# Kernel optimization log

Hardware: AMD Instinct MI355X
Metric: run time of the kernel (lower is better)

## Reference

```python
import jax, jax.numpy as jnp
import numpy as np

B, S, D, H, HD = 1, 4096, 768, 12, 64
L, C, WIN, NCLS = 2, 256, 256, 64
NC = S // C
V, FF = 50265, 3072
NEG = -1e9
SCALE = np.float32(1.0 / np.sqrt(HD))


def setup_inputs() -> dict:
    key = jax.random.key(0)
    ks = jax.random.split(key, 32)
    p = lambda k, shape: (0.02 * jax.random.normal(k, shape)).astype(jnp.float32)
    inp = {
        'x': jax.random.randint(ks[0], (B, S), 0, V, dtype=jnp.int32),
        'mask_src': jnp.ones((B, S), dtype=jnp.int32),
        'clss': jnp.sort(jax.random.randint(ks[1], (B, NCLS), 0, S, dtype=jnp.int32), axis=-1),
        'segs': jax.random.randint(ks[2], (B, S), 0, 2, dtype=jnp.int32),
        'word_emb': p(ks[3], (V, D)),
        'pos_emb': p(ks[4], (S, D)),
        'type_emb': p(ks[5], (2, D)),
        'ln_e_s': jnp.ones((D,), jnp.float32), 'ln_e_b': jnp.zeros((D,), jnp.float32),
        'Wq': p(ks[6], (L, D, D)), 'bq': jnp.zeros((L, D), jnp.float32),
        'Wk': p(ks[7], (L, D, D)), 'bk': jnp.zeros((L, D), jnp.float32),
        'Wv': p(ks[8], (L, D, D)), 'bv': jnp.zeros((L, D), jnp.float32),
        'Wqg': p(ks[9], (L, D, D)), 'bqg': jnp.zeros((L, D), jnp.float32),
        'Wkg': p(ks[10], (L, D, D)), 'bkg': jnp.zeros((L, D), jnp.float32),
        'Wvg': p(ks[11], (L, D, D)), 'bvg': jnp.zeros((L, D), jnp.float32),
        'Wo': p(ks[12], (L, D, D)), 'bo': jnp.zeros((L, D), jnp.float32),
        'ln1_s': jnp.ones((L, D), jnp.float32), 'ln1_b': jnp.zeros((L, D), jnp.float32),
        'Wf1': p(ks[13], (L, D, FF)), 'bf1': jnp.zeros((L, FF), jnp.float32),
        'Wf2': p(ks[14], (L, FF, D)), 'bf2': jnp.zeros((L, D), jnp.float32),
        'ln2_s': jnp.ones((L, D), jnp.float32), 'ln2_b': jnp.zeros((L, D), jnp.float32),
    }
    return inp


def _layer_norm(x, s, b):
    m = jnp.mean(x, -1, keepdims=True)
    v = jnp.mean((x - m) ** 2, -1, keepdims=True)
    return (x - m) * jax.lax.rsqrt(v + 1e-5) * s + b


def _forward(x, mask_src, clss, segs, word_emb, pos_emb, type_emb, ln_e_s, ln_e_b,
             Wq, bq, Wk, bk, Wv, bv, Wqg, bqg, Wkg, bkg, Wvg, bvg, Wo, bo,
             ln1_s, ln1_b, Wf1, bf1, Wf2, bf2, ln2_s, ln2_b):
    # global positions: union of all clss values, same for every batch row
    g_idx = clss.reshape(-1)                                       # [NCLS]
    is_glb = jnp.zeros((S,), bool).at[g_idx].set(True)             # [S]
    kvalid = (mask_src > 0) & (~is_glb)[None, :]                   # band keys: no pad, no global
    gi = (jnp.arange(NC) * C)[:, None] + jnp.arange(3 * C)[None, :]  # gather idx into padded seq
    rel = jnp.arange(3 * C)[None, :] - (jnp.arange(C)[:, None] + C)  # key offset from query
    band_ok = jnp.abs(rel) <= WIN                                   # [C,3C]
    kv3 = jnp.pad(kvalid, ((0, 0), (C, C)))[:, gi]                  # [B,NC,3C]
    bmask = band_ok[None, None, None, :, :] & kv3[:, None, :, None, :]  # [B,1,NC,C,3C]
    gkey_ok = (mask_src[:, g_idx] > 0)[:, None, None, :]            # [B,1,1,NCLS]
    full_ok = (mask_src > 0)[:, None, None, :]                      # [B,1,1,S]

    h = _layer_norm(word_emb[x] + pos_emb[jnp.arange(S)][None] + type_emb[segs], ln_e_s, ln_e_b)

    for l in range(L):
        q = ((h @ Wq[l] + bq[l]).reshape(B, S, H, HD)) * SCALE
        k = (h @ Wk[l] + bk[l]).reshape(B, S, H, HD)
        v = (h @ Wv[l] + bv[l]).reshape(B, S, H, HD)
        # --- sliding-window band attention ---
        k3 = jnp.pad(k, ((0, 0), (C, C), (0, 0), (0, 0)))[:, gi]    # [B,NC,3C,H,HD]
        v3 = jnp.pad(v, ((0, 0), (C, C), (0, 0), (0, 0)))[:, gi]
        qc = q.reshape(B, NC, C, H, HD)
        sb = jnp.einsum('bnqhd,bnkhd->bhnqk', qc, k3)               # [B,H,NC,C,3C]
        sb = jnp.where(bmask, sb, NEG)
        # --- global keys seen by every query ---
        kg, vg = k[:, g_idx], v[:, g_idx]                           # [B,NCLS,H,HD]
        sg = jnp.einsum('bshd,bkhd->bhsk', q, kg)                   # [B,H,S,NCLS]
        sg = jnp.where(gkey_ok, sg, NEG)
        scores = jnp.concatenate([sg, sb.reshape(B, H, S, 3 * C)], -1)
        probs = jax.nn.softmax(scores, axis=-1)
        pg = probs[..., :NCLS]
        pb = probs[..., NCLS:].reshape(B, H, NC, C, 3 * C)
        out = jnp.einsum('bhnqk,bnkhd->bnqhd', pb, v3).reshape(B, S, H, HD)
        out = out + jnp.einsum('bhsk,bkhd->bshd', pg, vg)
        # --- global query tokens: full attention with *_global projections ---
        hg = h[:, g_idx]                                            # [B,NCLS,D]
        qg = ((hg @ Wqg[l] + bqg[l]).reshape(B, NCLS, H, HD)) * SCALE
        kgf = (h @ Wkg[l] + bkg[l]).reshape(B, S, H, HD)
        vgf = (h @ Wvg[l] + bvg[l]).reshape(B, S, H, HD)
        sfull = jnp.einsum('bqhd,bkhd->bhqk', qg, kgf)              # [B,H,NCLS,S]
        sfull = jnp.where(full_ok, sfull, NEG)
        og = jnp.einsum('bhqk,bkhd->bqhd', jax.nn.softmax(sfull, -1), vgf)
        out = out.at[:, g_idx].set(og)
        # --- output proj, residual, LN, FFN ---
        attn_out = out.reshape(B, S, D) @ Wo[l] + bo[l]
        h = _layer_norm(h + attn_out, ln1_s[l], ln1_b[l])
        ff = jax.nn.gelu(h @ Wf1[l] + bf1[l]) @ Wf2[l] + bf2[l]
        h = _layer_norm(h + ff, ln2_s[l], ln2_b[l])
    return h


def reference(x, mask_src, clss, segs, word_emb, pos_emb, type_emb, ln_e_s, ln_e_b,
              Wq, bq, Wk, bk, Wv, bv, Wqg, bqg, Wkg, bkg, Wvg, bvg, Wo, bo,
              ln1_s, ln1_b, Wf1, bf1, Wf2, bf2, ln2_s, ln2_b):
    return _forward(x, mask_src, clss, segs, word_emb, pos_emb, type_emb, ln_e_s, ln_e_b,
                    Wq, bq, Wk, bk, Wv, bv, Wqg, bqg, Wkg, bkg, Wvg, bvg, Wo, bo,
                    ln1_s, ln1_b, Wf1, bf1, Wf2, bf2, ln2_s, ln2_b)
```

## Files before the change

kernel.cpp:

```cpp
#include <hip/hip_runtime.h>
#include <hip/hip_bf16.h>
#include <cstdint>

#define SEQ  4096
#define DIM  768
#define NH   12
#define HDIM 64
#define NLAYER 2
#define CHK  256
#define WINR 256
#define NCLS 64
#define NCHK 16
#define FFD  3072
#define QSCALE 0.125f
#define LOG2E 1.44269504f
#define QSC2 (QSCALE * LOG2E)
#define SD ((size_t)SEQ * DIM)
#define PS_LD 72
#define TK 64

typedef __attribute__((__vector_size__(16))) float floatx4;
typedef __attribute__((ext_vector_type(8))) __bf16 bf16x8;
typedef __attribute__((ext_vector_type(4))) __bf16 bf16x4;

__device__ __forceinline__ void async16(const void* g, void* l) {
    __builtin_amdgcn_global_load_lds(
        (const __attribute__((address_space(1))) uint32_t*)g,
        (__attribute__((address_space(3))) uint32_t*)l, 16, 0, 0);
}

__device__ __forceinline__ float gelu_f(float x) {
    float x3 = x * x * x;
    return 0.5f * x * (1.0f + tanhf(0.7978845608028654f * (x + 0.044715f * x3)));
}

__global__ __launch_bounds__(64) void set_rank_kernel(
    const int* __restrict__ clss, int* __restrict__ isglb, int* __restrict__ glb_rank)
{
    int t = threadIdx.x;
    int p = clss[t];
    isglb[p] = 1;
    glb_rank[p] = t;
}

__global__ __launch_bounds__(256) void embed_ln_kernel(
    const int* __restrict__ x, const int* __restrict__ segs,
    const float* __restrict__ word_emb, const float* __restrict__ pos_emb,
    const float* __restrict__ type_emb, const float* __restrict__ gs,
    const float* __restrict__ gb, float* __restrict__ h, __bf16* __restrict__ hb,
    int* __restrict__ isglb, int* __restrict__ grank)
{
    int wave = threadIdx.x >> 6, lane = threadIdx.x & 63;
    int s = blockIdx.x * 4 + wave;
    if (lane == 0) { isglb[s] = 0; grank[s] = -1; }
    int w = x[s], sg = segs[s];
    const float4* wp = (const float4*)(word_emb + (size_t)w * DIM);
    const float4* pp = (const float4*)(pos_emb + (size_t)s * DIM);
    const float4* tp = (const float4*)(type_emb + (size_t)sg * DIM);
    float4 v[3]; float lsum = 0.f;
    #pragma unroll
    for (int i = 0; i < 3; i++) {
        int d4 = lane + i * 64;
        float4 a = wp[d4], b = pp[d4], c = tp[d4];
        float4 r;
        r.x = a.x + b.x + c.x; r.y = a.y + b.y + c.y;
        r.z = a.z + b.z + c.z; r.w = a.w + b.w + c.w;
        v[i] = r; lsum += r.x + r.y + r.z + r.w;
    }
    #pragma unroll
    for (int st = 32; st > 0; st >>= 1) lsum += __shfl_xor(lsum, st);
    float mean = lsum * (1.0f / DIM);
    float lv = 0.f;
    #pragma unroll
    for (int i = 0; i < 3; i++) {
        float dx = v[i].x - mean, dy = v[i].y - mean, dz = v[i].z - mean, dw = v[i].w - mean;
        lv += dx * dx + dy * dy + dz * dz + dw * dw;
    }
    #pragma unroll
    for (int st = 32; st > 0; st >>= 1) lv += __shfl_xor(lv, st);
    float rstd = rsqrtf(lv * (1.0f / DIM) + 1e-5f);
    #pragma unroll
    for (int i = 0; i < 3; i++) {
        int d4 = lane + i * 64;
        float4 s4v = ((const float4*)gs)[d4], b4v = ((const float4*)gb)[d4];
        float4 o;
        o.x = (v[i].x - mean) * rstd * s4v.x + b4v.x;
        o.y = (v[i].y - mean) * rstd * s4v.y + b4v.y;
        o.z = (v[i].z - mean) * rstd * s4v.z + b4v.z;
        o.w = (v[i].w - mean) * rstd * s4v.w + b4v.w;
        ((float4*)(h + (size_t)s * DIM))[d4] = o;
        bf16x4 ob; ob[0] = (__bf16)o.x; ob[1] = (__bf16)o.y;
        ob[2] = (__bf16)o.z; ob[3] = (__bf16)o.w;
        *(bf16x4*)(hb + (size_t)s * DIM + (size_t)d4 * 4) = ob;
    }
}

__global__ __launch_bounds__(256) void add_ln_kernel(
    const float* __restrict__ h, const float* __restrict__ r,
    const float* __restrict__ gs, const float* __restrict__ gb,
    float* __restrict__ hout, __bf16* __restrict__ hb)
{
    int wave = threadIdx.x >> 6, lane = threadIdx.x & 63;
    int s = blockIdx.x * 4 + wave;
    const float4* hp = (const float4*)(h + (size_t)s * DIM);
    const float4* rp = (const float4*)(r + (size_t)s * DIM);
    float4 v[3]; float lsum = 0.f;
    #pragma unroll
    for (int i = 0; i < 3; i++) {
        int d4 = lane + i * 64;
        float4 a = hp[d4], b = rp[d4];
        float4 q;
        q.x = a.x + b.x; q.y = a.y + b.y; q.z = a.z + b.z; q.w = a.w + b.w;
        v[i] = q; lsum += q.x + q.y + q.z + q.w;
    }
    #pragma unroll
    for (int st = 32; st > 0; st >>= 1) lsum += __shfl_xor(lsum, st);
    float mean = lsum * (1.0f / DIM);
    float lv = 0.f;
    #pragma unroll
    for (int i = 0; i < 3; i++) {
        float dx = v[i].x - mean, dy = v[i].y - mean, dz = v[i].z - mean, dw = v[i].w - mean;
        lv += dx * dx + dy * dy + dz * dz + dw * dw;
    }
    #pragma unroll
    for (int st = 32; st > 0; st >>= 1) lv += __shfl_xor(lv, st);
    float rstd = rsqrtf(lv * (1.0f / DIM) + 1e-5f);
    #pragma unroll
    for (int i = 0; i < 3; i++) {
        int d4 = lane + i * 64;
        float4 s4v = ((const float4*)gs)[d4], b4v = ((const float4*)gb)[d4];
        float4 o;
        o.x = (v[i].x - mean) * rstd * s4v.x + b4v.x;
        o.y = (v[i].y - mean) * rstd * s4v.y + b4v.y;
        o.z = (v[i].z - mean) * rstd * s4v.z + b4v.z;
        o.w = (v[i].w - mean) * rstd * s4v.w + b4v.w;
        ((float4*)(hout + (size_t)s * DIM))[d4] = o;
        bf16x4 ob; ob[0] = (__bf16)o.x; ob[1] = (__bf16)o.y;
        ob[2] = (__bf16)o.z; ob[3] = (__bf16)o.w;
        *(bf16x4*)(hb + (size_t)s * DIM + (size_t)d4 * 4) = ob;
    }
}

struct TArgs { const float* p14[14]; const float* f1[2]; const float* f2[2]; };
#define DD_ ((size_t)DIM * DIM)
__global__ __launch_bounds__(256) void tpose_setup_kernel(
// ... 9 lines not shown
        const float* s = (j == 0) ? bq : (j == 1) ? bk : (j == 2) ? bv : (j == 3) ? bkg : bvg;
        bqkv[idx] = s[l * 768 + d];
        return;
    }
    const float* src; __bf16* dst; int K, N, bx, by;
    if (b < 8064) {
        int z = b / 576, rr = b % 576;
        src = ta.p14[z]; dst = Wbf + (size_t)z * DD_;
        K = 768; N = 768; bx = (rr % 24) * 32; by = (rr / 24) * 32;
    } else if (b < 12672) {
        int bb = b - 8064; int z = bb / 2304, rr = bb % 2304;
        src = ta.f1[z]; dst = Wbf + 14 * DD_ + (size_t)z * 4 * DD_;
        K = 768; N = 3072; bx = (rr % 96) * 32; by = (rr / 96) * 32;
    } else {
        int bb = b - 12672; int z = bb / 2304, rr = bb % 2304;
        src = ta.f2[z]; dst = Wbf + 22 * DD_ + (size_t)z * 4 * DD_;
        K = 3072; N = 768; bx = (rr % 24) * 32; by = (rr / 24) * 32;
    }
    __shared__ float tile[32][33];
    int tx = threadIdx.x & 31, ty = threadIdx.x >> 5;
    #pragma unroll
    for (int i = 0; i < 32; i += 8)
        tile[ty + i][tx] = src[(size_t)(by + ty + i) * N + bx + tx];
    __syncthreads();
    #pragma unroll
    for (int i = 0; i < 32; i += 8)
        dst[(size_t)(bx + ty + i) * K + by + tx] = (__bf16)tile[tx][ty + i];
}

template<int TMv, int TNv>
__global__ __launch_bounds__(256) void mfma_gemm_t(
    const __bf16* __restrict__ A, const __bf16* __restrict__ Bt,
    const float* __restrict__ bias, float* __restrict__ Cf,
    __bf16* __restrict__ Cb, int M, int N, int K, float scale, int act)
{
    constexpr int AM = TMv / 32, AN = TNv / 32;
    constexpr int LA = TMv / 32, LB = TNv / 32;
    __shared__ __align__(16) __bf16 As[TMv * TK];
    __shared__ __align__(16) __bf16 Bs[TNv * TK];
    int t = threadIdx.x;
    int wave = t >> 6, lane = t & 63;
    int bm = blockIdx.x * TMv, bn = blockIdx.y * TNv;
    int wm = (wave & 1) * (TMv / 2), wn = (wave >> 1) * (TNv / 2);

    floatx4 acc[AM][AN];
    #pragma unroll
    for (int i = 0; i < AM; i++)
        #pragma unroll
        for (int j = 0; j < AN; j++) { floatx4 z = {0.f,0.f,0.f,0.f}; acc[i][j] = z; }

    const int mrow = lane & 15, kq = (lane >> 4) * 8;
    const int tr8 = lane >> 3, c8 = lane & 7;
    const int scol = (c8 ^ tr8) * 8;
    const int swz = (lane & 7) << 3;
    const __bf16* aBase = A  + (size_t)(bm + wave * 8 + tr8) * K + scol;
    const __bf16* bBase = Bt + (size_t)(bn + wave * 8 + tr8) * K + scol;

    for (int k0 = 0; k0 < K; k0 += TK) {
        __syncthreads();
        #pragma unroll
        for (int i = 0; i < LA; i++)
            async16(aBase + k0 + (size_t)i * 32 * K, &As[(size_t)(i * 256 + wave * 64) * 8]);
        #pragma unroll
        for (int i = 0; i < LB; i++)
            async16(bBase + k0 + (size_t)i * 32 * K, &Bs[(size_t)(i * 256 + wave * 64) * 8]);
        __builtin_amdgcn_s_waitcnt(0x0f70);
        __syncthreads();
        #pragma unroll
        for (int ks = 0; ks < 2; ks++) {
            const int e = (ks * 32 + kq) ^ swz;
            bf16x8 af[AM], bfr[AN];
            #pragma unroll
            for (int mt = 0; mt < AM; mt++)
                af[mt] = *(const bf16x8*)&As[(wm + mt * 16 + mrow) * TK + e];
            #pragma unroll
            for (int nt = 0; nt < AN; nt++)
                bfr[nt] = *(const bf16x8*)&Bs[(wn + nt * 16 + mrow) * TK + e];
            #pragma unroll
            for (int mt = 0; mt < AM; mt++)
                #pragma unroll
                for (int nt = 0; nt < AN; nt++)
                    acc[mt][nt] = __builtin_amdgcn_mfma_f32_16x16x32_bf16(
                        af[mt], bfr[nt], acc[mt][nt], 0, 0, 0);
        }
    }

    int col_l = lane & 15, row_l = (lane >> 4) * 4;
    #pragma unroll
    for (int nt = 0; nt < AN; nt++) {
        int col = bn + wn + nt * 16 + col_l;
        float bs = bias[col];
        #pragma unroll
        for (int mt = 0; mt < AM; mt++) {
            floatx4 v = acc[mt][nt];
            int row0 = bm + wm + mt * 16 + row_l;
            #pragma unroll
            for (int rr = 0; rr < 4; rr++) {
                float o = (v[rr] + bs) * scale;
                if (act) o = gelu_f(o);
                if (Cf) Cf[(size_t)(row0 + rr) * N + col] = o;
                if (Cb) Cb[(size_t)(row0 + rr) * N + col] = (__bf16)o;
            }
        }
    }
}

__global__ __launch_bounds__(256) void mfma_gemm_proj(
    const __bf16* __restrict__ A, const __bf16* __restrict__ Bt,
    const float* __restrict__ bias,
    __bf16* __restrict__ qb, __bf16* __restrict__ kb,
    __bf16* __restrict__ vb, __bf16* __restrict__ vtg,
    __bf16* __restrict__ kgb, __bf16* __restrict__ vgt, int K)
{
    __shared__ __align__(16) __bf16 As[128 * TK];
    __shared__ __align__(16) __bf16 Bs[128 * TK];
    int t = threadIdx.x;
    int wave = t >> 6, lane = t & 63;
    int bm = blockIdx.x * 128, bn = blockIdx.y * 128;
    int wm = (wave & 1) * 64, wn = (wave >> 1) * 64;

    floatx4 acc[4][4];
    #pragma unroll
    for (int i = 0; i < 4; i++)
        #pragma unroll
        for (int j = 0; j < 4; j++) { floatx4 z = {0.f,0.f,0.f,0.f}; acc[i][j] = z; }

    const int mrow = lane & 15, kq = (lane >> 4) * 8;
    const int tr8 = lane >> 3, c8 = lane & 7;
    const int scol = (c8 ^ tr8) * 8;
    const int swz = (lane & 7) << 3;
    const __bf16* aBase = A  + (size_t)(bm + wave * 8 + tr8) * K + scol;
    const __bf16* bBase = Bt + (size_t)(bn + wave * 8 + tr8) * K + scol;

    for (int k0 = 0; k0 < K; k0 += TK) {
        __syncthreads();
        #pragma unroll
        for (int i = 0; i < 4; i++) {
            async16(aBase + k0 + (size_t)i * 32 * K, &As[(size_t)(i * 256 + wave * 64) * 8]);
            async16(bBase + k0 + (size_t)i * 32 * K, &Bs[(size_t)(i * 256 + wave * 64) * 8]);
        }
        __builtin_amdgcn_s_waitcnt(0x0f70);
        __syncthreads();
        #pragma unroll
        for (int ks = 0; ks < 2; ks++) {
            const int e = (ks * 32 + kq) ^ swz;
            bf16x8 af[4], bfr[4];
            #pragma unroll
            for (int mt = 0; mt < 4; mt++)
                af[mt] = *(const bf16x8*)&As[(wm + mt * 16 + mrow) * TK + e];
            #pragma unroll
            for (int nt = 0; nt < 4; nt++)
                bfr[nt] = *(const bf16x8*)&Bs[(wn + nt * 16 + mrow) * TK + e];
            #pragma unroll
            for (int mt = 0; mt < 4; mt++)
                #pragma unroll
                for (int nt = 0; nt < 4; nt++)
                    acc[mt][nt] = __builtin_amdgcn_mfma_f32_16x16x32_bf16(
                        af[mt], bfr[nt], acc[mt][nt], 0, 0, 0);
        }
    }

    int col_l = lane & 15, row_l = (lane >> 4) * 4;
    int seg = bn / 768;
    int colw_base = bn - seg * 768 + wn;
    float scl = (seg == 0) ? QSC2 : 1.0f;
    #pragma unroll
    for (int nt = 0; nt < 4; nt++) {
        int col = bn + wn + nt * 16 + col_l;
        int colw = colw_base + nt * 16 + col_l;
        float bs = bias[col];
        #pragma unroll
        for (int mt = 0; mt < 4; mt++) {
            floatx4 v = acc[mt][nt];
            int row0 = bm + wm + mt * 16 + row_l;
            __bf16 t4[4];
            #pragma unroll
            for (int rr = 0; rr < 4; rr++) t4[rr] = (__bf16)((v[rr] + bs) * scl);
            if (seg <= 2 || seg == 3) {
                __bf16* dst = (seg == 0) ? qb : (seg == 1) ? kb : (seg == 2) ? vb : kgb;
                #pragma unroll
                for (int rr = 0; rr < 4; rr++)
                    dst[(size_t)(row0 + rr) * 768 + colw] = t4[rr];
            }
            if (seg == 2)
                *(uint2*)&vtg[(size_t)colw * SEQ + row0] = *(uint2*)t4;
            if (seg == 4)
                *(uint2*)&vgt[(size_t)colw * SEQ + row0] = *(uint2*)t4;
        }
    }
}

__global__ __launch_bounds__(256) void qg_proj(
    const __bf16* __restrict__ hb, const __bf16* __restrict__ Bt,
    const int* __restrict__ clss, const float* __restrict__ bias,
    __bf16* __restrict__ out)
{
    __shared__ __align__(16) __bf16 As[64 * TK];
    __shared__ __align__(16) __bf16 Bs[128 * TK];
    int t = threadIdx.x;
    int wave = t >> 6, lane = t & 63;
    int bn = blockIdx.y * 128;
    int wm = (wave & 1) * 32, wn = (wave >> 1) * 64;

    const int mrow = lane & 15, kq = (lane >> 4) * 8;
    const int tr8 = lane >> 3, c8 = lane & 7;
    const int scol = (c8 ^ tr8) * 8;
    const int swz = (lane & 7) << 3;
    int arow0 = wave * 8 + tr8;
    int g0 = clss[arow0], g1 = clss[32 + arow0];
    const __bf16* a0 = hb + (size_t)g0 * DIM + scol;
    const __bf16* a1 = hb + (size_t)g1 * DIM + scol;
    const __bf16* bBase = Bt + (size_t)(bn + wave * 8 + tr8) * DIM + scol;

    floatx4 acc[2][4];
    #pragma unroll
    for (int i = 0; i < 2; i++)
        #pragma unroll
        for (int j = 0; j < 4; j++) { floatx4 z = {0.f,0.f,0.f,0.f}; acc[i][j] = z; }

    for (int k0 = 0; k0 < DIM; k0 += TK) {
        __syncthreads();
        async16(a0 + k0, &As[(size_t)(wave * 64) * 8]);
        async16(a1 + k0, &As[(size_t)(256 + wave * 64) * 8]);
        #pragma unroll
        for (int i = 0; i < 4; i++)
            async16(bBase + k0 + (size_t)i * 32 * DIM, &Bs[(size_t)(i * 256 + wave * 64) * 8]);
        __builtin_amdgcn_s_waitcnt(0x0f70);
        __syncthreads();
        #pragma unroll
        for (int ks = 0; ks < 2; ks++) {
            const int e = (ks * 32 + kq) ^ swz;
            bf16x8 af[2], bfr[4];
            #pragma unroll
            for (int mt = 0; mt < 2; mt++)
                af[mt] = *(const bf16x8*)&As[(wm + mt * 16 + mrow) * TK + e];
            #pragma unroll
            for (int nt = 0; nt < 4; nt++)
                bfr[nt] = *(const bf16x8*)&Bs[(wn + nt * 16 + mrow) * TK + e];
            #pragma unroll
            for (int mt = 0; mt < 2; mt++)
                #pragma unroll
                for (int nt = 0; nt < 4; nt++)
                    acc[mt][nt] = __builtin_amdgcn_mfma_f32_16x16x32_bf16(
                        af[mt], bfr[nt], acc[mt][nt], 0, 0, 0);
        }
    }
    int col_l = lane & 15, row_l = (lane >> 4) * 4;
    #pragma unroll
    for (int nt = 0; nt < 4; nt++) {
        int col = bn + wn + nt * 16 + col_l;
        float bs = bias[col];
        #pragma unroll
        for (int mt = 0; mt < 2; mt++) {
            floatx4 v = acc[mt][nt];
            int row0 = wm + mt * 16 + row_l;
            #pragma unroll
            for (int rr = 0; rr < 4; rr++)
                out[(size_t)(row0 + rr) * DIM + col] = (__bf16)((v[rr] + bs) * QSC2);
        }
    }
}

__global__ __launch_bounds__(256) void attn_kernel(
    const __bf16* __restrict__ qb, const __bf16* __restrict__ kb,
    const __bf16* __restrict__ vb, const __bf16* __restrict__ vtg,
    const __bf16* __restrict__ qgbb, const __bf16* __restrict__ kgb,
    const __bf16* __restrict__ vgt,
    const int* __restrict__ clss, const int* __restrict__ mask_src,
    const int* __restrict__ is_glb,
    float* __restrict__ OpartB, float* __restrict__ mlpartB,
    float* __restrict__ OpartG, float* __restrict__ mlpartG)
{
    __shared__ __align__(16) __bf16 Kt[4096];
    __shared__ __align__(16) __bf16 Vt[4096];
    __shared__ __align__(16) __bf16 Ps[4][32 * PS_LD];
    __shared__ int kvalid[64];
    __shared__ int gpos[64];

    const int hh = blockIdx.y;
    const int t = threadIdx.x, wave = t >> 6, lane = t & 63;
    const int quad = lane >> 4, col_l = lane & 15, row_l = quad * 4;
    const int l3 = lane & 3, l2h = lane >> 2, l7 = lane & 7, l3h = lane >> 3;
    __bf16* PsW = Ps[wave];

    if (blockIdx.z >= 4) {
        const int sp = blockIdx.x * 2 + (blockIdx.z - 4);
        bf16x8 aq[2];
        {
            const __bf16* qp = qgbb + (size_t)(wave * 16 + col_l) * DIM + hh * HDIM;
            aq[0] = *(const bf16x8*)(qp + quad * 8);
            aq[1] = *(const bf16x8*)(qp + 32 + quad * 8);
        }
        floatx4 oacc[4];
        #pragma unroll
        for (int i = 0; i < 4; i++) { floatx4 z = {0.f,0.f,0.f,0.f}; oacc[i] = z; }
        float m4[4], l4[4];
        #pragma unroll
        for (int r = 0; r < 4; r++) { m4[r] = -1e30f; l4[r] = 0.f; }

        for (int tt = 0; tt < 2; tt++) {
            int pos0 = sp * 128 + tt * 64;
            __syncthreads();
            if (t < 64) kvalid[t] = (mask_src[pos0 + t] > 0) ? 1 : 0;
            #pragma unroll
            for (int ii = 0; ii < 2; ii++) {
                int gid = wave * 2 + ii;
                int p = gid >> 2, kbase = (gid & 3) * 16;
                async16(kgb + (size_t)(pos0 + kbase + l2h) * DIM + hh * HDIM + p * 32 + l3 * 8,
                        &Kt[p * 2048 + kbase * 32]);
            }
            #pragma unroll
            for (int ii = 0; ii < 2; ii++) {
                int gid = wave * 2 + ii;
                int p = gid >> 2, dbase = (gid & 3) * 16;
                async16(vgt + (size_t)(hh * HDIM + dbase + l2h) * SEQ + pos0 + p * 32 + l3 * 8,
                        &Vt[p * 2048 + dbase * 32]);
            }
            __builtin_amdgcn_s_waitcnt(0x0f70);
            __syncthreads();
// ... 37 lines not shown
                rsum += __shfl_xor(rsum, 4);
                rsum += __shfl_xor(rsum, 8);
                l4[rr] = l4[rr] * alpha + rsum;
                m4[rr] = mn;
                #pragma unroll
                for (int nt = 0; nt < 4; nt++) oacc[nt][rr] *= alpha;
            }
            bf16x8 ap0 = *(const bf16x8*)&PsW[col_l * PS_LD + quad * 8];
            bf16x8 ap1 = *(const bf16x8*)&PsW[col_l * PS_LD + 32 + quad * 8];
            #pragma unroll
            for (int nt = 0; nt < 4; nt++) {
                bf16x8 b0 = *(const bf16x8*)&Vt[(nt * 16 + col_l) * 32 + quad * 8];
                bf16x8 b1 = *(const bf16x8*)&Vt[2048 + (nt * 16 + col_l) * 32 + quad * 8];
                oacc[nt] = __builtin_amdgcn_mfma_f32_16x16x32_bf16(ap0, b0, oacc[nt], 0,0,0);
                oacc[nt] = __builtin_amdgcn_mfma_f32_16x16x32_bf16(ap1, b1, oacc[nt], 0,0,0);
            }
        }
        size_t base = (size_t)(hh * 32 + sp) * 64;
        #pragma unroll
        for (int nt = 0; nt < 4; nt++)
            #pragma unroll
            for (int rr = 0; rr < 4; rr++)
                OpartG[(base + wave * 16 + row_l + rr) * 64 + nt * 16 + col_l] = oacc[nt][rr];
        if (col_l == 0) {
            #pragma unroll
            for (int rr = 0; rr < 4; rr++) {
                mlpartG[(base + wave * 16 + row_l + rr) * 2]     = m4[rr];
                mlpartG[(base + wave * 16 + row_l + rr) * 2 + 1] = l4[rr];
            }
        }
        return;
    }

    const int n = blockIdx.x, zi = blockIdx.z;
    const int qh = zi >> 1, ks = zi & 1;
    const int qw = qh * 128 + wave * 32;

    if (t < 64) gpos[t] = clss[t];

    bf16x8 aq[2][2];
    #pragma unroll
    for (int mt = 0; mt < 2; mt++) {
        const __bf16* qp = qb + (size_t)(n * CHK + qw + mt * 16 + col_l) * DIM + hh * HDIM;
        aq[mt][0] = *(const bf16x8*)(qp + quad * 8);
        aq[mt][1] = *(const bf16x8*)(qp + 32 + quad * 8);
    }

    floatx4 oacc[2][4];
    #pragma unroll
    for (int i = 0; i < 2; i++)
        #pragma unroll
        for (int j = 0; j < 4; j++) { floatx4 z = {0.f,0.f,0.f,0.f}; oacc[i][j] = z; }
    float mrw[8], lrw[8];
    #pragma unroll
    for (int r = 0; r < 8; r++) { mrw[r] = -1e30f; lrw[r] = 0.f; }

    const int ntiles = ks ? 5 : 6;

    for (int tt = 0; tt < ntiles; tt++) {
        __syncthreads();
        int jbase = -1;
        int isglob = (ks == 0 && tt == 0);
        if (isglob) {
            if (t < 64) kvalid[t] = (mask_src[gpos[t]] > 0) ? 1 : 0;
            #pragma unroll
            for (int g = 0; g < 2; g++) {
                int gid = wave * 2 + g;
                int p = gid >> 2, kbase = (gid & 3) * 16;
                int pos = gpos[kbase + l2h];
                async16(kb + (size_t)pos * DIM + hh * HDIM + p * 32 + l3 * 8,
                        &Kt[p * 2048 + kbase * 32]);
            }
            __bf16* Vrow = &Ps[0][0];
            #pragma unroll
            for (int g = 0; g < 2; g++) {
                int cg = wave * 2 + g;
                int pos = gpos[cg * 8 + l3h];
                async16(vb + (size_t)pos * DIM + hh * HDIM + l7 * 8,
                        &Vrow[cg * 64 * 8]);
            }
        } else {
            int jt = ks ? (qh * 2 + 5 + tt) : (qh * 2 + tt - 1);
            jbase = jt * 64;
            if (t < 64) {
                int pos = n * CHK + jbase + t - CHK;
                kvalid[t] = (pos >= 0 && pos < SEQ && mask_src[pos] > 0
                             && is_glb[pos] == 0) ? 1 : 0;
            }
            int s0 = n * CHK + jbase - CHK;
            #pragma unroll
            for (int g = 0; g < 2; g++) {
                int gid = wave * 2 + g;
                int p = gid >> 2, kbase = (gid & 3) * 16;
                int pos = s0 + kbase + l2h; pos = min(max(pos, 0), SEQ - 1);
                async16(kb + (size_t)pos * DIM + hh * HDIM + p * 32 + l3 * 8,
                        &Kt[p * 2048 + kbase * 32]);
            }
            #pragma unroll
            for (int g = 0; g < 2; g++) {
                int gid = wave * 2 + g;
                int p = gid >> 2, dbase = (gid & 3) * 16;
                int d = dbase + l2h;
                int s = s0 + p * 32 + l3 * 8; s = min(max(s, 0), SEQ - 8);
                async16(vtg + (size_t)(hh * HDIM + d) * SEQ + s,
                        &Vt[p * 2048 + dbase * 32]);
            }
        }
        __builtin_amdgcn_s_waitcnt(0x0f70);
        __syncthreads();
        if (isglob) {
            const __bf16* Vrow = &Ps[0][0];
            for (int idx = t; idx < 4096; idx += 256) {
                int key = idx >> 6, d = idx & 63;
                Vt[(key >> 5) * 2048 + d * 32 + (key & 31)] = Vrow[idx];
            }
// ... 59 lines not shown
                lrw[ri] = lrw[ri] * alpha + rsum;
                mrw[ri] = mn;
                #pragma unroll
                for (int nt = 0; nt < 4; nt++) oacc[mt][nt][rr] *= alpha;
            }
        }
        bf16x8 bvf[4][2], ap[2][2];
        #pragma unroll
        for (int nt = 0; nt < 4; nt++) {
            bvf[nt][0] = *(const bf16x8*)&Vt[(nt * 16 + col_l) * 32 + quad * 8];
            bvf[nt][1] = *(const bf16x8*)&Vt[2048 + (nt * 16 + col_l) * 32 + quad * 8];
        }
        #pragma unroll
        for (int mt = 0; mt < 2; mt++) {
            ap[mt][0] = *(const bf16x8*)&PsW[(mt * 16 + col_l) * PS_LD + quad * 8];
            ap[mt][1] = *(const bf16x8*)&PsW[(mt * 16 + col_l) * PS_LD + 32 + quad * 8];
        }
        #pragma unroll
        for (int mt = 0; mt < 2; mt++)
            #pragma unroll
            for (int nt = 0; nt < 4; nt++) {
                oacc[mt][nt] = __builtin_amdgcn_mfma_f32_16x16x32_bf16(
                    ap[mt][0], bvf[nt][0], oacc[mt][nt], 0,0,0);
                oacc[mt][nt] = __builtin_amdgcn_mfma_f32_16x16x32_bf16(
                    ap[mt][1], bvf[nt][1], oacc[mt][nt], 0,0,0);
            }
    }

    #pragma unroll
    for (int mt = 0; mt < 2; mt++) {
        #pragma unroll
        for (int rr = 0; rr < 4; rr++) {
            int srow = n * CHK + qw + mt * 16 + row_l + rr;
            size_t rbase = ((size_t)ks * SEQ + srow) * NH + hh;
            #pragma unroll
            for (int nt = 0; nt < 4; nt++)
                OpartB[rbase * 64 + nt * 16 + col_l] = oacc[mt][nt][rr];
            if (col_l == 0) {
                mlpartB[rbase * 2]     = mrw[mt * 4 + rr];
                mlpartB[rbase * 2 + 1] = lrw[mt * 4 + rr];
            }
        }
    }
}

__global__ __launch_bounds__(256) void attn_finalize(
    const float* __restrict__ OpartB, const float* __restrict__ mlpartB,
    const float* __restrict__ OpartG, const float* __restrict__ mlpartG,
    const int* __restrict__ glb_rank, __bf16* __restrict__ outb)
{
    int g = threadIdx.x >> 6, d = threadIdx.x & 63;
    int s = blockIdx.x * 4 + g, hh = blockIdx.y;
    int r = glb_rank[s];
    float o;
    if (r >= 0) {
        float M = -1e30f;
        for (int sp = 0; sp < 32; sp++)
            M = fmaxf(M, mlpartG[(((size_t)hh * 32 + sp) * 64 + r) * 2]);
        float L = 0.f, acc = 0.f;
        for (int sp = 0; sp < 32; sp++) {
            size_t b = ((size_t)hh * 32 + sp) * 64 + r;
            float w = exp2f(mlpartG[b * 2] - M);
            L += mlpartG[b * 2 + 1] * w;
            acc += w * OpartG[b * 64 + d];
        }
        o = acc / L;
    } else {
        size_t r0 = ((size_t)s) * NH + hh;
        size_t r1 = ((size_t)SEQ + s) * NH + hh;
        float m0 = mlpartB[r0 * 2], l0 = mlpartB[r0 * 2 + 1];
        float m1 = mlpartB[r1 * 2], l1 = mlpartB[r1 * 2 + 1];
        float M = fmaxf(m0, m1);
        float w0 = exp2f(m0 - M), w1 = exp2f(m1 - M);
        o = (OpartB[r0 * 64 + d] * w0 + OpartB[r1 * 64 + d] * w1) / (l0 * w0 + l1 * w1);
    }
    outb[(size_t)s * DIM + hh * HDIM + d] = (__bf16)o;
}

extern "C" void kernel_launch(void* const* d_in, const int* in_sizes, int n_in,
                              void* d_out, int out_size, void* d_ws, size_t ws_size,
                              hipStream_t stream)
{
    const int* x        = (const int*)d_in[0];
    const int* mask_src = (const int*)d_in[1];
    const int* clss     = (const int*)d_in[2];
    const int* segs     = (const int*)d_in[3];
    const float* word_emb = (const float*)d_in[4];
    const float* pos_emb  = (const float*)d_in[5];
    const float* type_emb = (const float*)d_in[6];
    const float* ln_e_s   = (const float*)d_in[7];
    const float* ln_e_b   = (const float*)d_in[8];
    const float* Wq  = (const float*)d_in[9];
    const float* bq  = (const float*)d_in[10];
    const float* Wk  = (const float*)d_in[11];
    const float* bk  = (const float*)d_in[12];
    const float* Wv  = (const float*)d_in[13];
    const float* bv  = (const float*)d_in[14];
    const float* Wqg = (const float*)d_in[15];
    const float* bqg = (const float*)d_in[16];
    const float* Wkg = (const float*)d_in[17];
    const float* bkg = (const float*)d_in[18];
    const float* Wvg = (const float*)d_in[19];
    const float* bvg = (const float*)d_in[20];
    const float* Wo  = (const float*)d_in[21];
    const float* bo  = (const float*)d_in[22];
    const float* ln1_s = (const float*)d_in[23];
    const float* ln1_b = (const float*)d_in[24];
    const float* Wf1 = (const float*)d_in[25];
    const float* bf1 = (const float*)d_in[26];
    const float* Wf2 = (const float*)d_in[27];
    const float* bf2 = (const float*)d_in[28];
    const float* ln2_s = (const float*)d_in[29];
    const float* ln2_b = (const float*)d_in[30];

    const size_t DD = (size_t)DIM * DIM;
    float* ws = (float*)d_ws;
    float*  h    = ws;
    float*  s4   = ws + SD;
    __bf16* hb   = (__bf16*)(ws + 2 * SD);
    __bf16* b6b  = (__bf16*)(ws + 2 * SD) + SD;
    __bf16* qb   = (__bf16*)(ws + 3 * SD);
    __bf16* kb   = (__bf16*)(ws + 3 * SD) + SD;
    __bf16* vb   = (__bf16*)(ws + 4 * SD);
    __bf16* vtg  = (__bf16*)(ws + 4 * SD) + SD;
    __bf16* kgb  = (__bf16*)(ws + 5 * SD);
    __bf16* vgt  = (__bf16*)(ws + 5 * SD) + SD;
    __bf16* gelu_b = qb;
    float* extra = ws + 6 * SD;
    __bf16* Wbf   = (__bf16*)extra;
    float* after_w = extra + 15 * DD;
    float* bqkv   = after_w;
    float* OpartG = bqkv + 7680;
    float* mlpartG= OpartG + 1572864;
    float* OpartB = mlpartG + 49152;
    float* mlpartB= OpartB + 6291456;
    __bf16* qgbb  = (__bf16*)(mlpartB + 196608);
    int*   isglb  = (int*)(qgbb + (size_t)NCLS * DIM);
    int*   grank  = isglb + SEQ;

    embed_ln_kernel<<<SEQ / 4, 256, 0, stream>>>(x, segs, word_emb, pos_emb, type_emb,
                                                 ln_e_s, ln_e_b, h, hb, isglb, grank);
    set_rank_kernel<<<1, 64, 0, stream>>>(clss, isglb, grank);
    {
        TArgs ta{};
        ta.p14[0] = Wq;        ta.p14[1] = Wk;        ta.p14[2] = Wv;
        ta.p14[3] = Wkg;       ta.p14[4] = Wvg;
        ta.p14[5] = Wq + DD;   ta.p14[6] = Wk + DD;   ta.p14[7] = Wv + DD;
        ta.p14[8] = Wkg + DD;  ta.p14[9] = Wvg + DD;
        ta.p14[10] = Wo;       ta.p14[11] = Wo + DD;
        ta.p14[12] = Wqg;      ta.p14[13] = Wqg + DD;
        ta.f1[0] = Wf1; ta.f1[1] = Wf1 + (size_t)DIM * FFD;
        ta.f2[0] = Wf2; ta.f2[1] = Wf2 + (size_t)FFD * DIM;
        tpose_setup_kernel<<<17310, 256, 0, stream>>>(ta, Wbf, bq, bk, bv, bkg, bvg, bqkv);
    }

    for (int l = 0; l < NLAYER; l++) {
        const float* bqg_l = bqg + (size_t)l * DIM;
        const float* bo_l  = bo  + (size_t)l * DIM;
        const float* bf1_l = bf1 + (size_t)l * FFD;
        const float* bf2_l = bf2 + (size_t)l * DIM;

        qg_proj<<<dim3(1, 6), 256, 0, stream>>>(
            hb, Wbf + 12 * DD + (size_t)l * DD, clss, bqg_l, qgbb);
        mfma_gemm_proj<<<dim3(SEQ / 128, 3840 / 128), 256, 0, stream>>>(
            hb, Wbf + (size_t)l * 5 * DD, bqkv + l * 3840,
            qb, kb, vb, vtg, kgb, vgt, DIM);
        attn_kernel<<<dim3(NCHK, NH, 6), 256, 0, stream>>>(
            qb, kb, vb, vtg, qgbb, kgb, vgt, clss, mask_src, isglb,
            OpartB, mlpartB, OpartG, mlpartG);
        attn_finalize<<<dim3(SEQ / 4, NH), 256, 0, stream>>>(
            OpartB, mlpartB, OpartG, mlpartG, grank, b6b);
        mfma_gemm_t<128, 64><<<dim3(SEQ / 128, DIM / 64), 256, 0, stream>>>(
            b6b, Wbf + 10 * DD + (size_t)l * DD, bo_l, s4, nullptr,
            SEQ, DIM, DIM, 1.0f, 0);
        add_ln_kernel<<<SEQ / 4, 256, 0, stream>>>(h, s4, ln1_s + (size_t)l * DIM,
                                                   ln1_b + (size_t)l * DIM, h, hb);
        mfma_gemm_t<128, 128><<<dim3(SEQ / 128, FFD / 128), 256, 0, stream>>>(
            hb, Wbf + 14 * DD + (size_t)l * 4 * DD, bf1_l, nullptr, gelu_b,
            SEQ, FFD, DIM, 1.0f, 1);
        mfma_gemm_t<128, 64><<<dim3(SEQ / 128, DIM / 64), 256, 0, stream>>>(
            gelu_b, Wbf + 22 * DD + (size_t)l * 4 * DD, bf2_l, s4, nullptr,
            SEQ, DIM, FFD, 1.0f, 0);
        add_ln_kernel<<<SEQ / 4, 256, 0, stream>>>(h, s4, ln2_s + (size_t)l * DIM,
                                                   ln2_b + (size_t)l * DIM,
                                                   (l == NLAYER - 1) ? (float*)d_out : h, hb);
    }
}
```

Before: 783.9 us.

## Split-K output/FFN2 GEMMs, fuse qg projection and band-attention finalize

The Wo and FFN2 GEMMs are split along K into two grid-z slices. Each slice writes its own fp32 partial, and the following add+LayerNorm kernel sums both partials, which doubles the block count for these narrow-N GEMMs. The separate qg_proj launch is folded into extra blockIdx.y columns of the QKV projection kernel. Band attention no longer splits key tiles across two blocks: each block normalizes its own output and writes bf16 directly, and only global-query rows go through a small finalize kernel. This removes launches and partial buffers, at the cost of fewer, longer attention blocks and an extra fp32 partial read in the LayerNorm kernels.

Result: faster. 721.8 us (-7.9%).

```diff
diff --git a/kernel.cpp b/kernel.cpp
--- a/kernel.cpp
+++ b/kernel.cpp
@@ -35,12 +35,9 @@
 }
 
 __global__ __launch_bounds__(64) void set_rank_kernel(
-    const int* __restrict__ clss, int* __restrict__ isglb, int* __restrict__ glb_rank)
+    const int* __restrict__ clss, int* __restrict__ isglb)
 {
-    int t = threadIdx.x;
-    int p = clss[t];
-    isglb[p] = 1;
-    glb_rank[p] = t;
+    isglb[clss[threadIdx.x]] = 1;
 }
 
 __global__ __launch_bounds__(256) void embed_ln_kernel(
@@ -48,11 +45,11 @@
     const float* __restrict__ word_emb, const float* __restrict__ pos_emb,
     const float* __restrict__ type_emb, const float* __restrict__ gs,
     const float* __restrict__ gb, float* __restrict__ h, __bf16* __restrict__ hb,
-    int* __restrict__ isglb, int* __restrict__ grank)
+    int* __restrict__ isglb)
 {
     int wave = threadIdx.x >> 6, lane = threadIdx.x & 63;
     int s = blockIdx.x * 4 + wave;
-    if (lane == 0) { isglb[s] = 0; grank[s] = -1; }
+    if (lane == 0) isglb[s] = 0;
     int w = x[s], sg = segs[s];
     const float4* wp = (const float4*)(word_emb + (size_t)w * DIM);
     const float4* pp = (const float4*)(pos_emb + (size_t)s * DIM);
@@ -97,6 +94,7 @@
 
 __global__ __launch_bounds__(256) void add_ln_kernel(
     const float* __restrict__ h, const float* __restrict__ r,
+    const float* __restrict__ r2,
     const float* __restrict__ gs, const float* __restrict__ gb,
     float* __restrict__ hout, __bf16* __restrict__ hb)
 {
@@ -104,13 +102,15 @@
     int s = blockIdx.x * 4 + wave;
     const float4* hp = (const float4*)(h + (size_t)s * DIM);
     const float4* rp = (const float4*)(r + (size_t)s * DIM);
+    const float4* rp2 = (const float4*)(r2 + (size_t)s * DIM);
     float4 v[3]; float lsum = 0.f;
     #pragma unroll
     for (int i = 0; i < 3; i++) {
         int d4 = lane + i * 64;
-        float4 a = hp[d4], b = rp[d4];
+        float4 a = hp[d4], b = rp[d4], c = rp2[d4];
         float4 q;
-        q.x = a.x + b.x; q.y = a.y + b.y; q.z = a.z + b.z; q.w = a.w + b.w;
+        q.x = a.x + b.x + c.x; q.y = a.y + b.y + c.y;
+        q.z = a.z + b.z + c.z; q.w = a.w + b.w + c.w;
         v[i] = q; lsum += q.x + q.y + q.z + q.w;
     }
     #pragma unroll
@@ -186,7 +186,8 @@
 __global__ __launch_bounds__(256) void mfma_gemm_t(
     const __bf16* __restrict__ A, const __bf16* __restrict__ Bt,
     const float* __restrict__ bias, float* __restrict__ Cf,
-    __bf16* __restrict__ Cb, int M, int N, int K, float scale, int act)
+    float* __restrict__ Cf2, __bf16* __restrict__ Cb,
+    int M, int N, int K, float scale, int act)
 {
     constexpr int AM = TMv / 32, AN = TNv / 32;
     constexpr int LA = TMv / 32, LB = TNv / 32;
@@ -196,6 +197,9 @@
     int wave = t >> 6, lane = t & 63;
     int bm = blockIdx.x * TMv, bn = blockIdx.y * TNv;
     int wm = (wave & 1) * (TMv / 2), wn = (wave >> 1) * (TNv / 2);
+    int kz = blockIdx.z;
+    int kn = K / (int)gridDim.z, kbeg = kz * kn;
+    float* Cfo = (kz == 0) ? Cf : Cf2;
 
     floatx4 acc[AM][AN];
     #pragma unroll
@@ -210,7 +214,7 @@
     const __bf16* aBase = A  + (size_t)(bm + wave * 8 + tr8) * K + scol;
     const __bf16* bBase = Bt + (size_t)(bn + wave * 8 + tr8) * K + scol;
 
-    for (int k0 = 0; k0 < K; k0 += TK) {
+    for (int k0 = kbeg; k0 < kbeg + kn; k0 += TK) {
         __syncthreads();
         #pragma unroll
         for (int i = 0; i < LA; i++)
@@ -243,7 +247,7 @@
     #pragma unroll
     for (int nt = 0; nt < AN; nt++) {
         int col = bn + wn + nt * 16 + col_l;
-        float bs = bias[col];
+        float bs = (kz == 0) ? bias[col] : 0.f;
         #pragma unroll
         for (int mt = 0; mt < AM; mt++) {
             floatx4 v = acc[mt][nt];
@@ -252,7 +256,7 @@
             for (int rr = 0; rr < 4; rr++) {
                 float o = (v[rr] + bs) * scale;
                 if (act) o = gelu_f(o);
-                if (Cf) Cf[(size_t)(row0 + rr) * N + col] = o;
+                if (Cfo) Cfo[(size_t)(row0 + rr) * N + col] = o;
                 if (Cb) Cb[(size_t)(row0 + rr) * N + col] = (__bf16)o;
             }
         }
@@ -264,25 +268,88 @@
     const float* __restrict__ bias,
     __bf16* __restrict__ qb, __bf16* __restrict__ kb,
     __bf16* __restrict__ vb, __bf16* __restrict__ vtg,
-    __bf16* __restrict__ kgb, __bf16* __restrict__ vgt, int K)
+    __bf16* __restrict__ kgb, __bf16* __restrict__ vgt, int K,
+    const __bf16* __restrict__ Wqg_bt, const float* __restrict__ bqg,
+    const int* __restrict__ clss, __bf16* __restrict__ qgbb)
 {
     __shared__ __align__(16) __bf16 As[128 * TK];
     __shared__ __align__(16) __bf16 Bs[128 * TK];
     int t = threadIdx.x;
     int wave = t >> 6, lane = t & 63;
-    int bm = blockIdx.x * 128, bn = blockIdx.y * 128;
-    int wm = (wave & 1) * 64, wn = (wave >> 1) * 64;
-
-    floatx4 acc[4][4];
-    #pragma unroll
-    for (int i = 0; i < 4; i++)
-        #pragma unroll
-        for (int j = 0; j < 4; j++) { floatx4 z = {0.f,0.f,0.f,0.f}; acc[i][j] = z; }
-
     const int mrow = lane & 15, kq = (lane >> 4) * 8;
     const int tr8 = lane >> 3, c8 = lane & 7;
     const int scol = (c8 ^ tr8) * 8;
     const int swz = (lane & 7) << 3;
+    int col_l = lane & 15, row_l = (lane >> 4) * 4;
+
+    if (blockIdx.y >= 30) {
+        if (blockIdx.x != 0) return;
+        int bn = (blockIdx.y - 30) * 128;
+        int wm = (wave & 1) * 32, wn = (wave >> 1) * 64;
+        int arow0 = wave * 8 + tr8;
+        int g0 = clss[arow0], g1 = clss[32 + arow0];
+        const __bf16* a0 = A + (size_t)g0 * DIM + scol;
+        const __bf16* a1 = A + (size_t)g1 * DIM + scol;
+        const __bf16* bBase = Wqg_bt + (size_t)(bn + wave * 8 + tr8) * DIM + scol;
+
+        floatx4 acc[2][4];
+        #pragma unroll
+        for (int i = 0; i < 2; i++)
+            #pragma unroll
+            for (int j = 0; j < 4; j++) { floatx4 z = {0.f,0.f,0.f,0.f}; acc[i][j] = z; }
+
+        for (int k0 = 0; k0 < DIM; k0 += TK) {
+            __syncthreads();
+            async16(a0 + k0, &As[(size_t)(wave * 64) * 8]);
+            async16(a1 + k0, &As[(size_t)(256 + wave * 64) * 8]);
+            #pragma unroll
+            for (int i = 0; i < 4; i++)
+                async16(bBase + k0 + (size_t)i * 32 * DIM, &Bs[(size_t)(i * 256 + wave * 64) * 8]);
+            __builtin_amdgcn_s_waitcnt(0x0f70);
+            __syncthreads();
+            #pragma unroll
+            for (int ks = 0; ks < 2; ks++) {
+                const int e = (ks * 32 + kq) ^ swz;
+                bf16x8 af[2], bfr[4];
+                #pragma unroll
+                for (int mt = 0; mt < 2; mt++)
+                    af[mt] = *(const bf16x8*)&As[(wm + mt * 16 + mrow) * TK + e];
+                #pragma unroll
+                for (int nt = 0; nt < 4; nt++)
+                    bfr[nt] = *(const bf16x8*)&Bs[(wn + nt * 16 + mrow) * TK + e];
+                #pragma unroll
+                for (int mt = 0; mt < 2; mt++)
+                    #pragma unroll
+                    for (int nt = 0; nt < 4; nt++)
+                        acc[mt][nt] = __builtin_amdgcn_mfma_f32_16x16x32_bf16(
+                            af[mt], bfr[nt], acc[mt][nt], 0, 0, 0);
+            }
+        }
+        #pragma unroll
+        for (int nt = 0; nt < 4; nt++) {
+            int col = bn + wn + nt * 16 + col_l;
+            float bs = bqg[col];
+            #pragma unroll
+            for (int mt = 0; mt < 2; mt++) {
+                floatx4 v = acc[mt][nt];
+                int row0 = wm + mt * 16 + row_l;
+                #pragma unroll
+                for (int rr = 0; rr < 4; rr++)
+                    qgbb[(size_t)(row0 + rr) * DIM + col] = (__bf16)((v[rr] + bs) * QSC2);
+            }
+        }
+        return;
+    }
+
+    int bm = blockIdx.x * 128, bn = blockIdx.y * 128;
+    int wm = (wave & 1) * 64, wn = (wave >> 1) * 64;
+
+    floatx4 acc[4][4];
+    #pragma unroll
+    for (int i = 0; i < 4; i++)
+        #pragma unroll
+        for (int j = 0; j < 4; j++) { floatx4 z = {0.f,0.f,0.f,0.f}; acc[i][j] = z; }
+
     const __bf16* aBase = A  + (size_t)(bm + wave * 8 + tr8) * K + scol;
     const __bf16* bBase = Bt + (size_t)(bn + wave * 8 + tr8) * K + scol;
 
@@ -314,7 +381,6 @@
         }
     }
 
-    int col_l = lane & 15, row_l = (lane >> 4) * 4;
     int seg = bn / 768;
     int colw_base = bn - seg * 768 + wn;
     float scl = (seg == 0) ? QSC2 : 1.0f;
@@ -340,77 +406,6 @@
                 *(uint2*)&vtg[(size_t)colw * SEQ + row0] = *(uint2*)t4;
             if (seg == 4)
                 *(uint2*)&vgt[(size_t)colw * SEQ + row0] = *(uint2*)t4;
-        }
-    }
-}
-
-__global__ __launch_bounds__(256) void qg_proj(
-    const __bf16* __restrict__ hb, const __bf16* __restrict__ Bt,
-    const int* __restrict__ clss, const float* __restrict__ bias,
-    __bf16* __restrict__ out)
-{
-    __shared__ __align__(16) __bf16 As[64 * TK];
-    __shared__ __align__(16) __bf16 Bs[128 * TK];
-    int t = threadIdx.x;
-    int wave = t >> 6, lane = t & 63;
-    int bn = blockIdx.y * 128;
-    int wm = (wave & 1) * 32, wn = (wave >> 1) * 64;
-
-    const int mrow = lane & 15, kq = (lane >> 4) * 8;
-    const int tr8 = lane >> 3, c8 = lane & 7;
-    const int scol = (c8 ^ tr8) * 8;
-    const int swz = (lane & 7) << 3;
-    int arow0 = wave * 8 + tr8;
-    int g0 = clss[arow0], g1 = clss[32 + arow0];
-    const __bf16* a0 = hb + (size_t)g0 * DIM + scol;
-    const __bf16* a1 = hb + (size_t)g1 * DIM + scol;
-    const __bf16* bBase = Bt + (size_t)(bn + wave * 8 + tr8) * DIM + scol;
-
-    floatx4 acc[2][4];
-    #pragma unroll
-    for (int i = 0; i < 2; i++)
-        #pragma unroll
-        for (int j = 0; j < 4; j++) { floatx4 z = {0.f,0.f,0.f,0.f}; acc[i][j] = z; }
-
-    for (int k0 = 0; k0 < DIM; k0 += TK) {
-        __syncthreads();
-        async16(a0 + k0, &As[(size_t)(wave * 64) * 8]);
-        async16(a1 + k0, &As[(size_t)(256 + wave * 64) * 8]);
-        #pragma unroll
-        for (int i = 0; i < 4; i++)
-            async16(bBase + k0 + (size_t)i * 32 * DIM, &Bs[(size_t)(i * 256 + wave * 64) * 8]);
-        __builtin_amdgcn_s_waitcnt(0x0f70);
-        __syncthreads();
-        #pragma unroll
-        for (int ks = 0; ks < 2; ks++) {
-            const int e = (ks * 32 + kq) ^ swz;
-            bf16x8 af[2], bfr[4];
-            #pragma unroll
-            for (int mt = 0; mt < 2; mt++)
-                af[mt] = *(const bf16x8*)&As[(wm + mt * 16 + mrow) * TK + e];
-            #pragma unroll
-            for (int nt = 0; nt < 4; nt++)
-                bfr[nt] = *(const bf16x8*)&Bs[(wn + nt * 16 + mrow) * TK + e];
-            #pragma unroll
-            for (int mt = 0; mt < 2; mt++)
-                #pragma unroll
-                for (int nt = 0; nt < 4; nt++)
-                    acc[mt][nt] = __builtin_amdgcn_mfma_f32_16x16x32_bf16(
-                        af[mt], bfr[nt], acc[mt][nt], 0, 0, 0);
-        }
-    }
-    int col_l = lane & 15, row_l = (lane >> 4) * 4;
-    #pragma unroll
-    for (int nt = 0; nt < 4; nt++) {
-        int col = bn + wn + nt * 16 + col_l;
-        float bs = bias[col];
-        #pragma unroll
-        for (int mt = 0; mt < 2; mt++) {
-            floatx4 v = acc[mt][nt];
-            int row0 = wm + mt * 16 + row_l;
-            #pragma unroll
-            for (int rr = 0; rr < 4; rr++)
-                out[(size_t)(row0 + rr) * DIM + col] = (__bf16)((v[rr] + bs) * QSC2);
         }
     }
 }
@@ -422,8 +417,8 @@
     const __bf16* __restrict__ vgt,
     const int* __restrict__ clss, const int* __restrict__ mask_src,
     const int* __restrict__ is_glb,
-    float* __restrict__ OpartB, float* __restrict__ mlpartB,
-    float* __restrict__ OpartG, float* __restrict__ mlpartG)
+    float* __restrict__ OpartG, float* __restrict__ mlpartG,
+    __bf16* __restrict__ outb)
 {
     __shared__ __align__(16) __bf16 Kt[4096];
     __shared__ __align__(16) __bf16 Vt[4096];
@@ -437,8 +432,8 @@
     const int l3 = lane & 3, l2h = lane >> 2, l7 = lane & 7, l3h = lane >> 3;
     __bf16* PsW = Ps[wave];
 
-    if (blockIdx.z >= 4) {
-        const int sp = blockIdx.x * 2 + (blockIdx.z - 4);
+    if (blockIdx.z >= 2) {
+        const int sp = blockIdx.x * 2 + (blockIdx.z - 2);
         bf16x8 aq[2];
         {
             const __bf16* qp = qgbb + (size_t)(wave * 16 + col_l) * DIM + hh * HDIM;
@@ -542,8 +537,7 @@
         return;
     }
 
-    const int n = blockIdx.x, zi = blockIdx.z;
-    const int qh = zi >> 1, ks = zi & 1;
+    const int n = blockIdx.x, qh = blockIdx.z;
     const int qw = qh * 128 + wave * 32;
 
     if (t < 64) gpos[t] = clss[t];
@@ -565,12 +559,10 @@
     #pragma unroll
     for (int r = 0; r < 8; r++) { mrw[r] = -1e30f; lrw[r] = 0.f; }
 
-    const int ntiles = ks ? 5 : 6;
-
-    for (int tt = 0; tt < ntiles; tt++) {
+    for (int tt = 0; tt < 11; tt++) {
         __syncthreads();
         int jbase = -1;
-        int isglob = (ks == 0 && tt == 0);
+        int isglob = (tt == 0);
         if (isglob) {
             if (t < 64) kvalid[t] = (mask_src[gpos[t]] > 0) ? 1 : 0;
             #pragma unroll
@@ -590,7 +582,7 @@
                         &Vrow[cg * 64 * 8]);
             }
         } else {
-            int jt = ks ? (qh * 2 + 5 + tt) : (qh * 2 + tt - 1);
+            int jt = qh * 2 + tt - 1;
             jbase = jt * 64;
             if (t < 64) {
                 int pos = n * CHK + jbase + t - CHK;
@@ -716,49 +708,33 @@
         #pragma unroll
         for (int rr = 0; rr < 4; rr++) {
             int srow = n * CHK + qw + mt * 16 + row_l + rr;
-            size_t rbase = ((size_t)ks * SEQ + srow) * NH + hh;
+            if (is_glb[srow]) continue;
+            float inv = 1.0f / lrw[mt * 4 + rr];
             #pragma unroll
             for (int nt = 0; nt < 4; nt++)
-                OpartB[rbase * 64 + nt * 16 + col_l] = oacc[mt][nt][rr];
-            if (col_l == 0) {
-                mlpartB[rbase * 2]     = mrw[mt * 4 + rr];
-                mlpartB[rbase * 2 + 1] = lrw[mt * 4 + rr];
-            }
-        }
-    }
-}
-
-__global__ __launch_bounds__(256) void attn_finalize(
-    const float* __restrict__ OpartB, const float* __restrict__ mlpartB,
+                outb[(size_t)srow * DIM + hh * HDIM + nt * 16 + col_l] =
+                    (__bf16)(oacc[mt][nt][rr] * inv);
+        }
+    }
+}
+
+__global__ __launch_bounds__(64) void gq_finalize(
     const float* __restrict__ OpartG, const float* __restrict__ mlpartG,
-    const int* __restrict__ glb_rank, __bf16* __restrict__ outb)
+    const int* __restrict__ clss, __bf16* __restrict__ outb)
 {
-    int g = threadIdx.x >> 6, d = threadIdx.x & 63;
-    int s = blockIdx.x * 4 + g, hh = blockIdx.y;
-    int r = glb_rank[s];
-    float o;
-    if (r >= 0) {
-        float M = -1e30f;
-        for (int sp = 0; sp < 32; sp++)
-            M = fmaxf(M, mlpartG[(((size_t)hh * 32 + sp) * 64 + r) * 2]);
-        float L = 0.f, acc = 0.f;
-        for (int sp = 0; sp < 32; sp++) {
-            size_t b = ((size_t)hh * 32 + sp) * 64 + r;
-            float w = exp2f(mlpartG[b * 2] - M);
-            L += mlpartG[b * 2 + 1] * w;
-            acc += w * OpartG[b * 64 + d];
-        }
-        o = acc / L;
-    } else {
-        size_t r0 = ((size_t)s) * NH + hh;
-        size_t r1 = ((size_t)SEQ + s) * NH + hh;
-        float m0 = mlpartB[r0 * 2], l0 = mlpartB[r0 * 2 + 1];
-        float m1 = mlpartB[r1 * 2], l1 = mlpartB[r1 * 2 + 1];
-        float M = fmaxf(m0, m1);
-        float w0 = exp2f(m0 - M), w1 = exp2f(m1 - M);
-        o = (OpartB[r0 * 64 + d] * w0 + OpartB[r1 * 64 + d] * w1) / (l0 * w0 + l1 * w1);
-    }
-    outb[(size_t)s * DIM + hh * HDIM + d] = (__bf16)o;
+    int r = blockIdx.x, hh = blockIdx.y, d = threadIdx.x;
+    float M = -1e30f;
+    for (int sp = 0; sp < 32; sp++)
+        M = fmaxf(M, mlpartG[(((size_t)hh * 32 + sp) * 64 + r) * 2]);
+    float L = 0.f, acc = 0.f;
+    for (int sp = 0; sp < 32; sp++) {
+        size_t b = ((size_t)hh * 32 + sp) * 64 + r;
+        float w = exp2f(mlpartG[b * 2] - M);
+        L += mlpartG[b * 2 + 1] * w;
+        acc += w * OpartG[b * 64 + d];
+    }
+    int pos = clss[r];
+    outb[(size_t)pos * DIM + hh * HDIM + d] = (__bf16)(acc / L);
 }
 
 extern "C" void kernel_launch(void* const* d_in, const int* in_sizes, int n_in,
@@ -816,15 +792,13 @@
     float* bqkv   = after_w;
     float* OpartG = bqkv + 7680;
     float* mlpartG= OpartG + 1572864;
-    float* OpartB = mlpartG + 49152;
-    float* mlpartB= OpartB + 6291456;
-    __bf16* qgbb  = (__bf16*)(mlpartB + 196608);
+    float* s4b    = mlpartG + 49152;
+    __bf16* qgbb  = (__bf16*)(s4b + SD);
     int*   isglb  = (int*)(qgbb + (size_t)NCLS * DIM);
-    int*   grank  = isglb + SEQ;
 
     embed_ln_kernel<<<SEQ / 4, 256, 0, stream>>>(x, segs, word_emb, pos_emb, type_emb,
-                                                 ln_e_s, ln_e_b, h, hb, isglb, grank);
-    set_rank_kernel<<<1, 64, 0, stream>>>(clss, isglb, grank);
+                                                 ln_e_s, ln_e_b, h, hb, isglb);
+    set_rank_kernel<<<1, 64, 0, stream>>>(clss, isglb);
     {
         TArgs ta{};
         ta.p14[0] = Wq;        ta.p14[1] = Wk;        ta.p14[2] = Wv;
@@ -844,28 +818,26 @@
         const float* bf1_l = bf1 + (size_t)l * FFD;
         const float* bf2_l = bf2 + (size_t)l * DIM;
 
-        qg_proj<<<dim3(1, 6), 256, 0, stream>>>(
-            hb, Wbf + 12 * DD + (size_t)l * DD, clss, bqg_l, qgbb);
-        mfma_gemm_proj<<<dim3(SEQ / 128, 3840 / 128), 256, 0, stream>>>(
+        mfma_gemm_proj<<<dim3(SEQ / 128, 36), 256, 0, stream>>>(
             hb, Wbf + (size_t)l * 5 * DD, bqkv + l * 3840,
-            qb, kb, vb, vtg, kgb, vgt, DIM);
-        attn_kernel<<<dim3(NCHK, NH, 6), 256, 0, stream>>>(
+            qb, kb, vb, vtg, kgb, vgt, DIM,
+            Wbf + 12 * DD + (size_t)l * DD, bqg_l, clss, qgbb);
+        attn_kernel<<<dim3(NCHK, NH, 4), 256, 0, stream>>>(
             qb, kb, vb, vtg, qgbb, kgb, vgt, clss, mask_src, isglb,
-            OpartB, mlpartB, OpartG, mlpartG);
-        attn_finalize<<<dim3(SEQ / 4, NH), 256, 0, stream>>>(
-            OpartB, mlpartB, OpartG, mlpartG, grank, b6b);
-        mfma_gemm_t<128, 64><<<dim3(SEQ / 128, DIM / 64), 256, 0, stream>>>(
-            b6b, Wbf + 10 * DD + (size_t)l * DD, bo_l, s4, nullptr,
+            OpartG, mlpartG, b6b);
+        gq_finalize<<<dim3(NCLS, NH), 64, 0, stream>>>(OpartG, mlpartG, clss, b6b);
+        mfma_gemm_t<128, 64><<<dim3(SEQ / 128, DIM / 64, 2), 256, 0, stream>>>(
+            b6b, Wbf + 10 * DD + (size_t)l * DD, bo_l, s4, s4b, nullptr,
             SEQ, DIM, DIM, 1.0f, 0);
-        add_ln_kernel<<<SEQ / 4, 256, 0, stream>>>(h, s4, ln1_s + (size_t)l * DIM,
+        add_ln_kernel<<<SEQ / 4, 256, 0, stream>>>(h, s4, s4b, ln1_s + (size_t)l * DIM,
                                                    ln1_b + (size_t)l * DIM, h, hb);
-        mfma_gemm_t<128, 128><<<dim3(SEQ / 128, FFD / 128), 256, 0, stream>>>(
-            hb, Wbf + 14 * DD + (size_t)l * 4 * DD, bf1_l, nullptr, gelu_b,
+        mfma_gemm_t<128, 128><<<dim3(SEQ / 128, FFD / 128, 1), 256, 0, stream>>>(
+            hb, Wbf + 14 * DD + (size_t)l * 4 * DD, bf1_l, nullptr, nullptr, gelu_b,
             SEQ, FFD, DIM, 1.0f, 1);
-        mfma_gemm_t<128, 64><<<dim3(SEQ / 128, DIM / 64), 256, 0, stream>>>(
-            gelu_b, Wbf + 22 * DD + (size_t)l * 4 * DD, bf2_l, s4, nullptr,
+        mfma_gemm_t<128, 64><<<dim3(SEQ / 128, DIM / 64, 2), 256, 0, stream>>>(
+            gelu_b, Wbf + 22 * DD + (size_t)l * 4 * DD, bf2_l, s4, s4b, nullptr,
             SEQ, DIM, FFD, 1.0f, 0);
-        add_ln_kernel<<<SEQ / 4, 256, 0, stream>>>(h, s4, ln2_s + (size_t)l * DIM,
+        add_ln_kernel<<<SEQ / 4, 256, 0, stream>>>(h, s4, s4b, ln2_s + (size_t)l * DIM,
                                                    ln2_b + (size_t)l * DIM,
                                                    (l == NLAYER - 1) ? (float*)d_out : h, hb);
     }
```
